# Kernel tuning notes

Measured on AMD Instinct MI355X. Metric: run time of the kernel, lower is better.

The kernel has to match this reference:

```python
import jax, jax.numpy as jnp
import numpy as np

C_IN = 256
GROUP = C_IN // 4  # module hard-codes group = C_in/4 -> 4 channels per group
EPS = 1e-5

@jax.custom_vjp
def binarize(x):
    # 1-bit quantization: sign forward, hardtanh straight-through backward
    return jnp.sign(x)

def _bin_fwd(x):
    return jnp.sign(x), x

def _bin_bwd(x, g):
    return (g * (jnp.abs(x) <= 1.0).astype(g.dtype),)

binarize.defvjp(_bin_fwd, _bin_bwd)

def channel_shuffle(x, g):
    # [N,C,H,W] -> [N,g,C/g,H,W] -> [N,C/g,g,H,W] -> [N,C,H,W]
    N, C, H, W = x.shape
    return x.reshape(N, g, C // g, H, W).transpose(0, 2, 1, 3, 4).reshape(N, C, H, W)


def setup_inputs() -> dict:
    key = jax.random.key(0)
    ks = jax.random.split(key, 6)
    x = jax.random.normal(ks[0], (32, C_IN, 56, 56), jnp.float32)
    # grouped conv weight: [C_out, C_in/group, kH, kW] = [256, 4, 3, 3]
    weight = jax.random.normal(ks[1], (C_IN, C_IN // GROUP, 3, 3), jnp.float32) * 0.1
    gamma = 1.0 + 0.1 * jax.random.normal(ks[2], (C_IN,), jnp.float32)
    beta = 0.1 * jax.random.normal(ks[3], (C_IN,), jnp.float32)
    running_mean = 0.1 * jax.random.normal(ks[4], (C_IN,), jnp.float32)
    running_var = jax.random.uniform(ks[5], (C_IN,), jnp.float32, 0.5, 1.5)
    return dict(x=x, weight=weight, gamma=gamma, beta=beta,
                running_mean=running_mean, running_var=running_var)


def reference(x, weight, gamma, beta, running_mean, running_var):
    # BatchNorm2d (inference-mode, affine=True)
    inv = gamma * jax.lax.rsqrt(running_var + EPS)
    xb = x * inv[None, :, None, None] + (beta - running_mean * inv)[None, :, None, None]
    # Conv2d_1w1a: binarize activations and weights, grouped 3x3 conv, no bias
    a = binarize(xb)
    w = binarize(weight)
    out = jax.lax.conv_general_dilated(
        a, w,
        window_strides=(1, 1),
        padding=((1, 1), (1, 1)),
        dimension_numbers=('NCHW', 'OIHW', 'NCHW'),
        feature_group_count=GROUP,
    )
    out = channel_shuffle(out, GROUP)
    # stride == 1 -> shortcut is identity
    return out + x
```

## Files before the change

### kernel.cpp

```cpp
#include <hip/hip_runtime.h>
#include <stdint.h>

#define H 56
#define W 56
#define HW (H * W)
#define CIN 256
#define NGRP 64
#define IMG (CIN * HW)
#define EPS 1e-5f

#define TS 58
#define TSTRIDE 64

__device__ __forceinline__ float mul_rn(float a, float b) {
    float d;
    asm("v_mul_f32 %0, %1, %2" : "=v"(d) : "v"(a), "v"(b));
    return d;
}
__device__ __forceinline__ float add_rn(float a, float b) {
    float d;
    asm("v_add_f32 %0, %1, %2" : "=v"(d) : "v"(a), "v"(b));
    return d;
}
__device__ __forceinline__ float sub_rn(float a, float b) {
    float d;
    asm("v_sub_f32 %0, %1, %2" : "=v"(d) : "v"(a), "v"(b));
    return d;
}

__global__ void pack_weights_kernel(const float* __restrict__ w,
                                    uint32_t* __restrict__ wb) {
    int c = blockIdx.x * blockDim.x + threadIdx.x;
    if (c >= CIN) return;
    uint32_t slo = 0, shi = 0, zlo = 0, zhi = 0;
    const float* wc = w + c * 36;
    for (int ci = 0; ci < 4; ++ci) {
        for (int t = 0; t < 9; ++t) {
            int b = t * 4 + ci;
            float v = wc[ci * 9 + t];
            uint32_t s = (v > 0.f) ? 1u : 0u;
            uint32_t z = (v != 0.f) ? 1u : 0u;
            if (b < 32) { slo |= s << b;       zlo |= z << b; }
            else        { shi |= s << (b-32);  zhi |= z << (b-32); }
        }
    }
    wb[c * 4]     = slo;
    wb[c * 4 + 1] = shi;
    wb[c * 4 + 2] = zlo;
    wb[c * 4 + 3] = zhi;
}

__global__ __launch_bounds__(256)
void binconv_kernel(const float* __restrict__ X,
                    const uint32_t* __restrict__ wb,
                    const float* __restrict__ gamma,
                    const float* __restrict__ beta,
                    const float* __restrict__ mean,
                    const float* __restrict__ var,
                    float* __restrict__ out) {
    __shared__ uint8_t tile_s[TS * TSTRIDE];
    __shared__ uint8_t tile_z[TS * TSTRIDE];

    const int bx  = blockIdx.x;
    const int n   = bx >> 6;
    const int g   = bx & 63;
    const int tid = threadIdx.x;

    float inv[4], bias[4];
#pragma unroll
    for (int ci = 0; ci < 4; ++ci) {
        int c = g * 4 + ci;
        float s  = sqrtf(var[c] + EPS);
        float r  = 1.0f / s;
        float iv = mul_rn(gamma[c], r);
        inv[ci]  = iv;
        bias[ci] = sub_rn(beta[c], mul_rn(mean[c], iv));
    }

    const float* Xn = X + (size_t)n * IMG;

    for (int p = tid; p < TS * TS; p += 256) {
        int y  = p / TS;
        int xx = p - y * TS;
        int hy = y - 1, wx = xx - 1;
        uint32_t sn = 0, zn = 0;
        if ((unsigned)hy < (unsigned)H && (unsigned)wx < (unsigned)W) {
            int off = hy * W + wx;
#pragma unroll
            for (int ci = 0; ci < 4; ++ci) {
                float v = Xn[(g * 4 + ci) * HW + off];
                float t = add_rn(mul_rn(v, inv[ci]), bias[ci]);
                sn |= (t > 0.f  ? 1u : 0u) << ci;
                zn |= (t != 0.f ? 1u : 0u) << ci;
            }
        }
        tile_s[y * TSTRIDE + xx] = (uint8_t)sn;
        tile_z[y * TSTRIDE + xx] = (uint8_t)zn;
    }

    uint32_t wslo[4], wshi[4], wzlo[4], wzhi[4];
#pragma unroll
    for (int j = 0; j < 4; ++j) {
        const uint32_t* p4 = &wb[(g * 4 + j) * 4];
        wslo[j] = p4[0]; wshi[j] = p4[1]; wzlo[j] = p4[2]; wzhi[j] = p4[3];
    }

    __syncthreads();

    for (int p = tid; p < HW; p += 256) {
        int h = p / W;
        int w = p - h * W;

        const int base = h * TSTRIDE + w;
        const uint8_t* s0 = &tile_s[base];
        const uint8_t* z0 = &tile_z[base];

        uint32_t r0s = (uint32_t)s0[0] | ((uint32_t)s0[1] << 4) | ((uint32_t)s0[2] << 8);
        uint32_t r1s = (uint32_t)s0[TSTRIDE]   | ((uint32_t)s0[TSTRIDE+1]   << 4) | ((uint32_t)s0[TSTRIDE+2]   << 8);
        uint32_t r2s = (uint32_t)s0[2*TSTRIDE] | ((uint32_t)s0[2*TSTRIDE+1] << 4) | ((uint32_t)s0[2*TSTRIDE+2] << 8);
        uint32_t r0z = (uint32_t)z0[0] | ((uint32_t)z0[1] << 4) | ((uint32_t)z0[2] << 8);
        uint32_t r1z = (uint32_t)z0[TSTRIDE]   | ((uint32_t)z0[TSTRIDE+1]   << 4) | ((uint32_t)z0[TSTRIDE+2]   << 8);
        uint32_t r2z = (uint32_t)z0[2*TSTRIDE] | ((uint32_t)z0[2*TSTRIDE+1] << 4) | ((uint32_t)z0[2*TSTRIDE+2] << 8);

        uint32_t alo = r0s | (r1s << 12) | ((r2s & 0xFFu) << 24);
        uint32_t ahi = r2s >> 8;
        uint32_t zlo = r0z | (r1z << 12) | ((r2z & 0xFFu) << 24);
        uint32_t zhi = r2z >> 8;

        float res[4];
#pragma unroll
        for (int j = 0; j < 4; ++j) {
            uint32_t ml = zlo & wzlo[j];
            uint32_t mh = zhi & wzhi[j];
            int vb = __popc(ml) + __popc(mh);
            int pc = __popc((alo ^ wslo[j]) & ml) + __popc((ahi ^ wshi[j]) & mh);
            res[j] = (float)(vb - 2 * pc);
        }

        size_t obase = (size_t)n * IMG + (size_t)p;
#pragma unroll
        for (int j = 0; j < 4; ++j) {
            size_t idx = obase + (size_t)(j * 64 + g) * HW;
            out[idx] = add_rn(res[j], X[idx]);
        }
    }
}

extern "C" void kernel_launch(void* const* d_in, const int* in_sizes, int n_in,
                              void* d_out, int out_size, void* d_ws, size_t ws_size,
                              hipStream_t stream) {
    const float* X     = (const float*)d_in[0];
    const float* Wt    = (const float*)d_in[1];
    const float* gamma = (const float*)d_in[2];
    const float* beta  = (const float*)d_in[3];
    const float* mean  = (const float*)d_in[4];
    const float* var   = (const float*)d_in[5];
    float* out = (float*)d_out;
    uint32_t* wb = (uint32_t*)d_ws;

    int N = in_sizes[0] / IMG;

    pack_weights_kernel<<<1, 256, 0, stream>>>(Wt, wb);
    binconv_kernel<<<N * NGRP, 256, 0, stream>>>(X, wb, gamma, beta, mean, var, out);
}
```

Before: 207.9 us.

## Bit-pack activation tile per row, vectorize loads/stores, fold weight packing in-kernel

Replaces the per-pixel byte tile with a row-wise bit-packed tile (4 bits per pixel, 8 words per row) filled with float4 loads, so each thread handles 4 output pixels and 4 output channels with popcount over 12-bit row windows. The residual and output use float4 loads and stores. Weight packing moves into the conv kernel, which removes the separate launch, and a fast path skips the weight zero-mask when all weights are nonzero. The intent is to cut global load/store instruction count and shared-memory traffic in this memory-bound kernel. In exchange it adds bit-shift work and a divergent edge case for the first column group.

```diff
diff --git a/kernel.cpp b/kernel.cpp
--- a/kernel.cpp
+++ b/kernel.cpp
@@ -5,66 +5,56 @@
 #define W 56
 #define HW (H * W)
 #define CIN 256
-#define NGRP 64
 #define IMG (CIN * HW)
 #define EPS 1e-5f
 
-#define TS 58
-#define TSTRIDE 64
+#define ROWW 8
+#define TROWS 58
 
 __device__ __forceinline__ float mul_rn(float a, float b) {
-    float d;
-    asm("v_mul_f32 %0, %1, %2" : "=v"(d) : "v"(a), "v"(b));
-    return d;
+    float d; asm("v_mul_f32 %0, %1, %2" : "=v"(d) : "v"(a), "v"(b)); return d;
 }
 __device__ __forceinline__ float add_rn(float a, float b) {
-    float d;
-    asm("v_add_f32 %0, %1, %2" : "=v"(d) : "v"(a), "v"(b));
-    return d;
+    float d; asm("v_add_f32 %0, %1, %2" : "=v"(d) : "v"(a), "v"(b)); return d;
 }
 __device__ __forceinline__ float sub_rn(float a, float b) {
-    float d;
-    asm("v_sub_f32 %0, %1, %2" : "=v"(d) : "v"(a), "v"(b));
-    return d;
-}
-
-__global__ void pack_weights_kernel(const float* __restrict__ w,
-                                    uint32_t* __restrict__ wb) {
-    int c = blockIdx.x * blockDim.x + threadIdx.x;
-    if (c >= CIN) return;
-    uint32_t slo = 0, shi = 0, zlo = 0, zhi = 0;
-    const float* wc = w + c * 36;
-    for (int ci = 0; ci < 4; ++ci) {
-        for (int t = 0; t < 9; ++t) {
-            int b = t * 4 + ci;
-            float v = wc[ci * 9 + t];
-            uint32_t s = (v > 0.f) ? 1u : 0u;
-            uint32_t z = (v != 0.f) ? 1u : 0u;
-            if (b < 32) { slo |= s << b;       zlo |= z << b; }
-            else        { shi |= s << (b-32);  zhi |= z << (b-32); }
-        }
-    }
-    wb[c * 4]     = slo;
-    wb[c * 4 + 1] = shi;
-    wb[c * 4 + 2] = zlo;
-    wb[c * 4 + 3] = zhi;
+    float d; asm("v_sub_f32 %0, %1, %2" : "=v"(d) : "v"(a), "v"(b)); return d;
 }
 
 __global__ __launch_bounds__(256)
 void binconv_kernel(const float* __restrict__ X,
-                    const uint32_t* __restrict__ wb,
+                    const float* __restrict__ Wt,
                     const float* __restrict__ gamma,
                     const float* __restrict__ beta,
                     const float* __restrict__ mean,
                     const float* __restrict__ var,
                     float* __restrict__ out) {
-    __shared__ uint8_t tile_s[TS * TSTRIDE];
-    __shared__ uint8_t tile_z[TS * TSTRIDE];
+    __shared__ uint32_t s_tile[TROWS * ROWW];
+    __shared__ uint32_t z_tile[TROWS * ROWW];
+    __shared__ uint32_t ws_l[4][3];
+    __shared__ uint32_t wz_l[4][3];
 
     const int bx  = blockIdx.x;
     const int n   = bx >> 6;
     const int g   = bx & 63;
     const int tid = threadIdx.x;
+
+    for (int i = tid; i < TROWS * ROWW; i += 256) { s_tile[i] = 0u; z_tile[i] = 0u; }
+
+    if (tid < 4) {
+        const float* wc = Wt + (size_t)(g * 4 + tid) * 36;
+        for (int r = 0; r < 3; ++r) {
+            uint32_t s = 0, z = 0;
+            for (int ci = 0; ci < 4; ++ci)
+                for (int kw = 0; kw < 3; ++kw) {
+                    float v = wc[ci * 9 + r * 3 + kw];
+                    int b = kw * 4 + ci;
+                    s |= (v > 0.f  ? 1u : 0u) << b;
+                    z |= (v != 0.f ? 1u : 0u) << b;
+                }
+            ws_l[tid][r] = s; wz_l[tid][r] = z;
+        }
+    }
 
     float inv[4], bias[4];
 #pragma unroll
@@ -77,71 +67,129 @@
         bias[ci] = sub_rn(beta[c], mul_rn(mean[c], iv));
     }
 
+    __syncthreads();
+
     const float* Xn = X + (size_t)n * IMG;
 
-    for (int p = tid; p < TS * TS; p += 256) {
-        int y  = p / TS;
-        int xx = p - y * TS;
-        int hy = y - 1, wx = xx - 1;
-        uint32_t sn = 0, zn = 0;
-        if ((unsigned)hy < (unsigned)H && (unsigned)wx < (unsigned)W) {
-            int off = hy * W + wx;
-#pragma unroll
-            for (int ci = 0; ci < 4; ++ci) {
-                float v = Xn[(g * 4 + ci) * HW + off];
-                float t = add_rn(mul_rn(v, inv[ci]), bias[ci]);
-                sn |= (t > 0.f  ? 1u : 0u) << ci;
-                zn |= (t != 0.f ? 1u : 0u) << ci;
-            }
-        }
-        tile_s[y * TSTRIDE + xx] = (uint8_t)sn;
-        tile_z[y * TSTRIDE + xx] = (uint8_t)zn;
-    }
-
-    uint32_t wslo[4], wshi[4], wzlo[4], wzhi[4];
-#pragma unroll
-    for (int j = 0; j < 4; ++j) {
-        const uint32_t* p4 = &wb[(g * 4 + j) * 4];
-        wslo[j] = p4[0]; wshi[j] = p4[1]; wzlo[j] = p4[2]; wzhi[j] = p4[3];
+    for (int task = tid; task < 56 * 14; task += 256) {
+        int r  = task / 14;
+        int cg = task - r * 14;
+        int off = r * W + cg * 4;
+        uint32_t s16 = 0, z16 = 0;
+#pragma unroll
+        for (int ci = 0; ci < 4; ++ci) {
+            const float4 v = *reinterpret_cast<const float4*>(
+                Xn + (size_t)(g * 4 + ci) * HW + off);
+            float t0 = add_rn(mul_rn(v.x, inv[ci]), bias[ci]);
+            float t1 = add_rn(mul_rn(v.y, inv[ci]), bias[ci]);
+            float t2 = add_rn(mul_rn(v.z, inv[ci]), bias[ci]);
+            float t3 = add_rn(mul_rn(v.w, inv[ci]), bias[ci]);
+            s16 |= ((t0 > 0.f ? 1u : 0u) << ci)        | ((t1 > 0.f ? 1u : 0u) << (4 + ci))
+                 | ((t2 > 0.f ? 1u : 0u) << (8 + ci))  | ((t3 > 0.f ? 1u : 0u) << (12 + ci));
+            z16 |= ((t0 != 0.f ? 1u : 0u) << ci)       | ((t1 != 0.f ? 1u : 0u) << (4 + ci))
+                 | ((t2 != 0.f ? 1u : 0u) << (8 + ci)) | ((t3 != 0.f ? 1u : 0u) << (12 + ci));
+        }
+        reinterpret_cast<uint16_t*>(&s_tile[(r + 1) * ROWW])[cg] = (uint16_t)s16;
+        reinterpret_cast<uint16_t*>(&z_tile[(r + 1) * ROWW])[cg] = (uint16_t)z16;
     }
 
     __syncthreads();
 
-    for (int p = tid; p < HW; p += 256) {
-        int h = p / W;
-        int w = p - h * W;
-
-        const int base = h * TSTRIDE + w;
-        const uint8_t* s0 = &tile_s[base];
-        const uint8_t* z0 = &tile_z[base];
-
-        uint32_t r0s = (uint32_t)s0[0] | ((uint32_t)s0[1] << 4) | ((uint32_t)s0[2] << 8);
-        uint32_t r1s = (uint32_t)s0[TSTRIDE]   | ((uint32_t)s0[TSTRIDE+1]   << 4) | ((uint32_t)s0[TSTRIDE+2]   << 8);
-        uint32_t r2s = (uint32_t)s0[2*TSTRIDE] | ((uint32_t)s0[2*TSTRIDE+1] << 4) | ((uint32_t)s0[2*TSTRIDE+2] << 8);
-        uint32_t r0z = (uint32_t)z0[0] | ((uint32_t)z0[1] << 4) | ((uint32_t)z0[2] << 8);
-        uint32_t r1z = (uint32_t)z0[TSTRIDE]   | ((uint32_t)z0[TSTRIDE+1]   << 4) | ((uint32_t)z0[TSTRIDE+2]   << 8);
-        uint32_t r2z = (uint32_t)z0[2*TSTRIDE] | ((uint32_t)z0[2*TSTRIDE+1] << 4) | ((uint32_t)z0[2*TSTRIDE+2] << 8);
-
-        uint32_t alo = r0s | (r1s << 12) | ((r2s & 0xFFu) << 24);
-        uint32_t ahi = r2s >> 8;
-        uint32_t zlo = r0z | (r1z << 12) | ((r2z & 0xFFu) << 24);
-        uint32_t zhi = r2z >> 8;
-
-        float res[4];
+    uint32_t wsj[4][3], wzj[4][3];
+    bool full = true;
+#pragma unroll
+    for (int j = 0; j < 4; ++j)
+#pragma unroll
+        for (int r = 0; r < 3; ++r) {
+            wsj[j][r] = ws_l[j][r];
+            wzj[j][r] = wz_l[j][r];
+            full = full && (wzj[j][r] == 0xFFFu);
+        }
+
+    float* On = out + (size_t)n * IMG;
+
+    for (int task = tid; task < 56 * 14; task += 256) {
+        int h  = task / 14;
+        int cg = task - h * 14;
+        int w0 = cg * 4;
+
+        uint64_t vs[3], vz[3];
+        int off;
+        if (w0 == 0) {
+            off = 0;
+#pragma unroll
+            for (int r = 0; r < 3; ++r) {
+                int base = (h + r) * ROWW;
+                vs[r] = (((uint64_t)s_tile[base] | ((uint64_t)s_tile[base + 1] << 32)) << 4);
+                vz[r] = (((uint64_t)z_tile[base] | ((uint64_t)z_tile[base + 1] << 32)) << 4);
+            }
+        } else {
+            int st = 4 * w0 - 4;
+            int i0 = st >> 5;
+            off = st & 31;
+#pragma unroll
+            for (int r = 0; r < 3; ++r) {
+                int base = (h + r) * ROWW + i0;
+                vs[r] = ((uint64_t)s_tile[base] | ((uint64_t)s_tile[base + 1] << 32));
+                vz[r] = ((uint64_t)z_tile[base] | ((uint64_t)z_tile[base + 1] << 32));
+            }
+        }
+
+        int res[4][4];
+        if (full) {
+#pragma unroll
+            for (int k = 0; k < 4; ++k) {
+                int sh = off + 4 * k;
+                uint32_t s0 = (uint32_t)(vs[0] >> sh) & 0xFFFu;
+                uint32_t s1 = (uint32_t)(vs[1] >> sh) & 0xFFFu;
+                uint32_t s2 = (uint32_t)(vs[2] >> sh) & 0xFFFu;
+                uint32_t z0 = (uint32_t)(vz[0] >> sh) & 0xFFFu;
+                uint32_t z1 = (uint32_t)(vz[1] >> sh) & 0xFFFu;
+                uint32_t z2 = (uint32_t)(vz[2] >> sh) & 0xFFFu;
+                int vb = __popc(z0) + __popc(z1) + __popc(z2);
+#pragma unroll
+                for (int j = 0; j < 4; ++j) {
+                    int pc = __popc((s0 ^ wsj[j][0]) & z0)
+                           + __popc((s1 ^ wsj[j][1]) & z1)
+                           + __popc((s2 ^ wsj[j][2]) & z2);
+                    res[j][k] = vb - 2 * pc;
+                }
+            }
+        } else {
+#pragma unroll
+            for (int k = 0; k < 4; ++k) {
+                int sh = off + 4 * k;
+                uint32_t s0 = (uint32_t)(vs[0] >> sh) & 0xFFFu;
+                uint32_t s1 = (uint32_t)(vs[1] >> sh) & 0xFFFu;
+                uint32_t s2 = (uint32_t)(vs[2] >> sh) & 0xFFFu;
+                uint32_t z0 = (uint32_t)(vz[0] >> sh) & 0xFFFu;
+                uint32_t z1 = (uint32_t)(vz[1] >> sh) & 0xFFFu;
+                uint32_t z2 = (uint32_t)(vz[2] >> sh) & 0xFFFu;
+#pragma unroll
+                for (int j = 0; j < 4; ++j) {
+                    uint32_t m0 = z0 & wzj[j][0];
+                    uint32_t m1 = z1 & wzj[j][1];
+                    uint32_t m2 = z2 & wzj[j][2];
+                    int vb = __popc(m0) + __popc(m1) + __popc(m2);
+                    int pc = __popc((s0 ^ wsj[j][0]) & m0)
+                           + __popc((s1 ^ wsj[j][1]) & m1)
+                           + __popc((s2 ^ wsj[j][2]) & m2);
+                    res[j][k] = vb - 2 * pc;
+                }
+            }
+        }
+
+        size_t pbase = (size_t)h * W + w0;
 #pragma unroll
         for (int j = 0; j < 4; ++j) {
-            uint32_t ml = zlo & wzlo[j];
-            uint32_t mh = zhi & wzhi[j];
-            int vb = __popc(ml) + __popc(mh);
-            int pc = __popc((alo ^ wslo[j]) & ml) + __popc((ahi ^ wshi[j]) & mh);
-            res[j] = (float)(vb - 2 * pc);
-        }
-
-        size_t obase = (size_t)n * IMG + (size_t)p;
-#pragma unroll
-        for (int j = 0; j < 4; ++j) {
-            size_t idx = obase + (size_t)(j * 64 + g) * HW;
-            out[idx] = add_rn(res[j], X[idx]);
+            size_t cofs = (size_t)(j * 64 + g) * HW + pbase;
+            const float4 sc = *reinterpret_cast<const float4*>(Xn + cofs);
+            float4 o;
+            o.x = add_rn((float)res[j][0], sc.x);
+            o.y = add_rn((float)res[j][1], sc.y);
+            o.z = add_rn((float)res[j][2], sc.z);
+            o.w = add_rn((float)res[j][3], sc.w);
+            *reinterpret_cast<float4*>(On + cofs) = o;
         }
     }
 }
@@ -156,10 +204,8 @@
     const float* mean  = (const float*)d_in[4];
     const float* var   = (const float*)d_in[5];
     float* out = (float*)d_out;
-    uint32_t* wb = (uint32_t*)d_ws;
 
     int N = in_sizes[0] / IMG;
 
-    pack_weights_kernel<<<1, 256, 0, stream>>>(Wt, wb);
-    binconv_kernel<<<N * NGRP, 256, 0, stream>>>(X, wb, gamma, beta, mean, var, out);
-}
+    binconv_kernel<<<N * 64, 256, 0, stream>>>(X, Wt, gamma, beta, mean, var, out);
+}
```

New measurement: 205.1 us. About the same (-1.4%).
